# Performance work log

Measured on AMD Instinct MI355X. Metric: run time of the kernel, lower is better.

Reference implementation:

```python
import jax, jax.numpy as jnp
import numpy as np

D_MODEL = 1024
N_HEADS_Q = 16
N_HEADS_KV = 4
D_HEAD = 64  # d_qk = d_v
THETA = 10000.0
CLAMP = 80.0


def apply_rope(x, theta=THETA):
    # x: (b, h, s, d) with d even; interleaved-pair rotary embedding
    b, h, s, d = x.shape
    inv_freq = 1.0 / (theta ** (jnp.arange(0, d, 2, dtype=jnp.float32) / d))  # (d/2,)
    ang = jnp.arange(s, dtype=jnp.float32)[:, None] * inv_freq[None, :]       # (s, d/2)
    cos, sin = jnp.cos(ang), jnp.sin(ang)
    x1, x2 = x[..., 0::2], x[..., 1::2]
    o1 = x1 * cos - x2 * sin
    o2 = x1 * sin + x2 * cos
    return jnp.stack([o1, o2], axis=-1).reshape(b, h, s, d).astype(x.dtype)


def setup_inputs() -> dict:
    key = jax.random.key(0)
    k0, k1, k2, k3, k4 = jax.random.split(key, 5)
    scale = 1.0 / np.sqrt(D_MODEL)
    return {
        "x": jax.random.normal(k0, (2, 2048, D_MODEL), dtype=jnp.float32),
        "Wq": jax.random.normal(k1, (N_HEADS_Q * D_HEAD, D_MODEL), dtype=jnp.float32) * scale,
        "Wk": jax.random.normal(k2, (N_HEADS_KV * D_HEAD, D_MODEL), dtype=jnp.float32) * scale,
        "Wv": jax.random.normal(k3, (N_HEADS_KV * D_HEAD, D_MODEL), dtype=jnp.float32) * scale,
        "Wo": jax.random.normal(k4, (D_MODEL, N_HEADS_Q * D_HEAD), dtype=jnp.float32) * scale,
    }


def _attention(x, Wq, Wk, Wv, Wo):
    b, s, _ = x.shape
    r = N_HEADS_Q // N_HEADS_KV  # queries per KV group
    # projections (Linear: y = x @ W^T, no bias)
    Q = (x @ Wq.T).reshape(b, s, N_HEADS_Q, D_HEAD).transpose(0, 2, 1, 3)   # (b, Hq, s, d)
    K = (x @ Wk.T).reshape(b, s, N_HEADS_KV, D_HEAD).transpose(0, 2, 1, 3)  # (b, Hkv, s, d)
    V = (x @ Wv.T).reshape(b, s, N_HEADS_KV, D_HEAD).transpose(0, 2, 1, 3)
    Q = apply_rope(Q)
    K = apply_rope(K)
    # GQA grouping: (b, Hkv, r, s, d)
    Qg = Q.reshape(b, N_HEADS_KV, r, s, D_HEAD)
    scores = jnp.einsum('bgrqd,bgkd->bgrqk', Qg, K)          # (b, g, r, s, s)
    scores = jnp.clip(scores, -CLAMP, CLAMP)
    causal = jnp.tril(jnp.ones((s, s), dtype=bool))
    scores = jnp.where(causal, scores, -jnp.inf)
    weights = jax.nn.softmax(scores / jnp.sqrt(jnp.float32(D_HEAD)), axis=-1)
    attn = jnp.einsum('bgrqk,bgkd->bgrqd', weights, V)       # (b, g, r, s, d)
    # '... h_kv r s d -> ... s (h_kv r d)'
    attn = attn.transpose(0, 3, 1, 2, 4).reshape(b, s, N_HEADS_Q * D_HEAD)
    return attn @ Wo.T


def reference(x, Wq, Wk, Wv, Wo):
    return _attention(x, Wq, Wk, Wv, Wo)
```

## Files before the change

kernel.cpp:

```cpp
#include <hip/hip_runtime.h>
#include <hip/hip_bf16.h>
#include <math.h>

typedef __attribute__((ext_vector_type(8))) short bf16x8;
typedef __attribute__((ext_vector_type(4))) float f32x4;

#define B_   2
#define S_   2048
#define DM   1024
#define HQ   16
#define HKV  4
#define DH   64

#define MFMA16(a, b, c) __builtin_amdgcn_mfma_f32_16x16x32_bf16(a, b, c, 0, 0, 0)

__device__ __forceinline__ void load_lds16(const __hip_bfloat16* g, __hip_bfloat16* l)
{
    __builtin_amdgcn_global_load_lds(
        (const __attribute__((address_space(1))) unsigned int*)g,
        (__attribute__((address_space(3))) unsigned int*)l, 16, 0, 0);
}

#define CVT_TOTAL 6815744
__global__ void cvt_all(const float* __restrict__ x,  const float* __restrict__ wq,
                        const float* __restrict__ wk, const float* __restrict__ wv,
                        const float* __restrict__ wo,
                        __hip_bfloat16* __restrict__ xb,  __hip_bfloat16* __restrict__ wqb,
                        __hip_bfloat16* __restrict__ wkb, __hip_bfloat16* __restrict__ wvb,
                        __hip_bfloat16* __restrict__ wob)
{
    int i = (blockIdx.x * blockDim.x + threadIdx.x) * 4;
    if (i >= CVT_TOTAL) return;
    const float* src; __hip_bfloat16* dst; int off;
    if      (i < 4194304) { src = x;  dst = xb;  off = 0; }
    else if (i < 5242880) { src = wq; dst = wqb; off = 4194304; }
    else if (i < 5505024) { src = wk; dst = wkb; off = 5242880; }
    else if (i < 5767168) { src = wv; dst = wvb; off = 5505024; }
    else                  { src = wo; dst = wob; off = 5767168; }
    i -= off;
    float4 v = *(const float4*)(src + i);
    union { ushort4 u; __hip_bfloat16 h[4]; } p;
    p.h[0] = __float2bfloat16(v.x);
    p.h[1] = __float2bfloat16(v.y);
    p.h[2] = __float2bfloat16(v.z);
    p.h[3] = __float2bfloat16(v.w);
    *(ushort4*)(dst + i) = p.u;
}

template <bool QKV>
__global__ __launch_bounds__(256, 3) void gemm_tile(
    const __hip_bfloat16* __restrict__ A,
    const __hip_bfloat16* __restrict__ W,
    float* __restrict__ C0, __hip_bfloat16* __restrict__ Qb,
    __hip_bfloat16* __restrict__ Kb, __hip_bfloat16* __restrict__ Vt, int K)
{
    const int wave = threadIdx.x >> 6;
    const int lane = threadIdx.x & 63;
    const int quad = lane >> 4;
    const int l16  = lane & 15;
    const int wm = wave >> 1, wn = wave & 1;
    const int m0 = blockIdx.x * 64;
    const int n0 = blockIdx.y * 128;

    __shared__ __align__(16) __hip_bfloat16 As[2][64 * 64];
    __shared__ __align__(16) __hip_bfloat16 Bs[2][128 * 64];

    f32x4 acc[2][4] = {};

    auto stage = [&](int sb, int kk) {
        #pragma unroll
        for (int r = 0; r < 6; ++r) {
            const int m = wave * 6 + r;
            if (m < 8) {
                const int g = (m << 6) | lane;
                const int row = g >> 3;
                const int cbs = ((g & 7) - row) & 7;
                load_lds16(A + (size_t)(m0 + row) * K + kk + cbs * 8,
                           &As[sb][m * 512]);
            } else {
                const int g = ((m - 8) << 6) | lane;
                const int row = g >> 3;
                const int cbs = ((g & 7) - row) & 7;
                load_lds16(W + (size_t)(n0 + row) * K + kk + cbs * 8,
                           &Bs[sb][(m - 8) * 512]);
            }
        }
    };

    const int NT = K >> 6;
    stage(0, 0);
    __syncthreads();

    for (int t = 0; t < NT; ++t) {
        const int buf = t & 1;
        if (t + 1 < NT) stage(buf ^ 1, (t + 1) << 6);
        #pragma unroll
        for (int ks = 0; ks < 2; ++ks) {
            bf16x8 af[2], bf[4];
            #pragma unroll
            for (int i = 0; i < 2; ++i) {
                const int ra = wm * 32 + i * 16 + l16;
                af[i] = *(const bf16x8*)
                    &As[buf][ra * 64 + ((ks * 4 + quad + ra) & 7) * 8];
            }
            #pragma unroll
            for (int j = 0; j < 4; ++j) {
                const int rb = wn * 64 + j * 16 + l16;
                bf[j] = *(const bf16x8*)
                    &Bs[buf][rb * 64 + ((ks * 4 + quad + rb) & 7) * 8];
            }
            #pragma unroll
            for (int i = 0; i < 2; ++i)
                #pragma unroll
                for (int j = 0; j < 4; ++j)
                    acc[i][j] = MFMA16(af[i], bf[j], acc[i][j]);
        }
        __syncthreads();
    }

    #pragma unroll
    for (int j = 0; j < 4; ++j) {
        const int cbase = n0 + wn * 64 + j * 16;
        const int cb = cbase + l16;
        if (QKV && cbase < 1280) {
            const int ii = (cb >> 1) & 31;
            const float f = exp2f((float)ii * -0.41524101186092f);
            const float f_rev = f * 0.15915494309189535f;
            const bool odd = cb & 1;
            #pragma unroll
            for (int i = 0; i < 2; ++i) {
                #pragma unroll
                for (int reg = 0; reg < 4; ++reg) {
                    const int row = m0 + wm * 32 + i * 16 + quad * 4 + reg;
                    const float v = acc[i][j][reg];
                    const float p = __shfl_xor(v, 1);
                    float rev = (float)(row & (S_ - 1)) * f_rev;
                    rev -= floorf(rev);
                    const float sn = __builtin_amdgcn_sinf(rev);
                    const float cs = __builtin_amdgcn_cosf(rev);
                    const float o = odd ? (p * sn + v * cs) : (v * cs - p * sn);
                    if (cbase < 1024)
                        Qb[(size_t)row * 1024 + cb] = __float2bfloat16(o);
                    else
                        Kb[(size_t)row * 256 + cb - 1024] = __float2bfloat16(o);
                }
            }
        } else {
            #pragma unroll
            for (int i = 0; i < 2; ++i) {
                #pragma unroll
                for (int reg = 0; reg < 4; ++reg) {
                    const int row = m0 + wm * 32 + i * 16 + quad * 4 + reg;
                    const float v = acc[i][j][reg];
                    if (QKV)
                        Vt[((size_t)(row >> 11) * 256 + (cb - 1280)) * S_ +
                           (row & (S_ - 1))] = __float2bfloat16(v);
                    else
                        C0[(size_t)row * 1024 + cb] = v;
                }
            }
        }
    }
}

template <bool MASKED>
__device__ __forceinline__ void softmax_store(
    const f32x4* sacc, int q, int k0, int quad, int l16,
    float& lsum, __hip_bfloat16* PsTile)
{
    #pragma unroll
    for (int nt = 0; nt < 4; ++nt) {
        union { ushort4 u; __hip_bfloat16 h[4]; } pk;
        #pragma unroll
        for (int reg = 0; reg < 4; ++reg) {
            const float sc = fminf(fmaxf(sacc[nt][reg], -80.0f), 80.0f);
            float p = exp2f(fmaf(sc, 0.18033688011112042f,
                                 -14.426950408889634f));
            if (MASKED) {
                const int key = k0 + nt * 16 + quad * 4 + reg;
                p = (key <= q) ? p : 0.0f;
            }
            lsum += p;
            pk.h[reg] = __float2bfloat16(p);
        }
        *(ushort4*)&PsTile[l16 * 72 + nt * 16 + quad * 4] = pk.u;
    }
}

__global__ __launch_bounds__(256, 2) void attn_mfma(
    const __hip_bfloat16* __restrict__ Q,
    const __hip_bfloat16* __restrict__ K,
    const __hip_bfloat16* __restrict__ Vt,
    __hip_bfloat16* __restrict__ ctx)
{
    const int t    = blockIdx.x & 15;
    const int hq   = (blockIdx.x >> 4) & (HQ - 1);
    const int b    = blockIdx.x >> 8;
    const int hkv  = hq >> 2;
    const int wave = threadIdx.x >> 6;
    const int lane = threadIdx.x & 63;
    const int quad = lane >> 4;
    const int l16  = lane & 15;

    const int qlo = t * 64 + wave * 16 + l16;
    const int qhi = (31 - t) * 64 + wave * 16 + l16;

    __shared__ __align__(16) __hip_bfloat16 Ks[2][64 * 64];
    __shared__ __align__(16) __hip_bfloat16 Vs[2][64 * 64];
    __shared__ __align__(16) __hip_bfloat16 Ps[4][2][16 * 72];

    const __hip_bfloat16* qpl = Q + ((size_t)(b * S_) + qlo) * (HQ * DH) + hq * DH + quad * 8;
    const __hip_bfloat16* qph = Q + ((size_t)(b * S_) + qhi) * (HQ * DH) + hq * DH + quad * 8;
    bf16x8 ql0 = *(const bf16x8*)qpl;
    bf16x8 ql1 = *(const bf16x8*)(qpl + 32);
    bf16x8 qh0 = *(const bf16x8*)qph;
    bf16x8 qh1 = *(const bf16x8*)(qph + 32);

    const __hip_bfloat16* Kg = K + (size_t)(b * S_) * (HKV * DH) + hkv * DH;
    const __hip_bfloat16* Vg = Vt + (size_t)(b * HKV + hkv) * DH * S_;

    auto stage = [&](int sb, int k0s) {
        #pragma unroll
        for (int r = 0; r < 2; ++r) {
            const int m = wave * 2 + r;
            const int g = m * 64 + lane;
            const int row = g >> 3;
            const int cbs = ((g & 7) - row) & 7;
            load_lds16(Kg + (size_t)(k0s + row) * (HKV * DH) + cbs * 8, &Ks[sb][m * 512]);
            load_lds16(Vg + (size_t)row * S_ + k0s + cbs * 8, &Vs[sb][m * 512]);
        }
    };

    stage(0, 0);

    float lsum_lo = 0.0f, lsum_hi = 0.0f;
    f32x4 Olo[4] = {}, Ohi[4] = {};
    const f32x4 zro = {0.0f, 0.0f, 0.0f, 0.0f};

    const int last = 31 - t;
    for (int kt = 0; kt <= last; ++kt) {
        const int buf = kt & 1;
        const int k0 = kt * 64;
        __syncthreads();
        if (kt < last) stage(buf ^ 1, k0 + 64);
        const bool dual = (kt <= t);

        bf16x8 ka[4][2];
        #pragma unroll
        for (int nt = 0; nt < 4; ++nt) {
            const int key = nt * 16 + l16;
            ka[nt][0] = *(const bf16x8*)&Ks[buf][key * 64 + ((quad + key) & 7) * 8];
            ka[nt][1] = *(const bf16x8*)&Ks[buf][key * 64 + ((quad + 4 + key) & 7) * 8];
        }
        f32x4 shi[4], slo[4];
        __builtin_amdgcn_s_setprio(1);
        #pragma unroll
        for (int nt = 0; nt < 4; ++nt) {
            shi[nt] = MFMA16(ka[nt][0], qh0, zro);
            shi[nt] = MFMA16(ka[nt][1], qh1, shi[nt]);
        }
        if (dual) {
            #pragma unroll
            for (int nt = 0; nt < 4; ++nt) {
                slo[nt] = MFMA16(ka[nt][0], ql0, zro);
                slo[nt] = MFMA16(ka[nt][1], ql1, slo[nt]);
            }
        }
        __builtin_amdgcn_s_setprio(0);

        if (kt == last) softmax_store<true >(shi, qhi, k0, quad, l16, lsum_hi, &Ps[wave][1][0]);
        else            softmax_store<false>(shi, qhi, k0, quad, l16, lsum_hi, &Ps[wave][1][0]);
        if (dual) {
            if (kt == t) softmax_store<true >(slo, qlo, k0, quad, l16, lsum_lo, &Ps[wave][0][0]);
            else         softmax_store<false>(slo, qlo, k0, quad, l16, lsum_lo, &Ps[wave][0][0]);
        }
        __asm__ __volatile__("s_waitcnt lgkmcnt(0)" ::: "memory");

        bf16x8 va[2][4];
        #pragma unroll
        for (int ks = 0; ks < 2; ++ks)
            #pragma unroll
            for (int dt = 0; dt < 4; ++dt) {
                const int d = dt * 16 + l16;
                va[ks][dt] = *(const bf16x8*)
                    &Vs[buf][d * 64 + ((ks * 4 + quad + d) & 7) * 8];
            }
        __builtin_amdgcn_s_setprio(1);
        #pragma unroll
        for (int ks = 0; ks < 2; ++ks) {
            bf16x8 pb = *(const bf16x8*)&Ps[wave][1][l16 * 72 + ks * 32 + quad * 8];
            #pragma unroll
            for (int dt = 0; dt < 4; ++dt)
                Ohi[dt] = MFMA16(va[ks][dt], pb, Ohi[dt]);
        }
        if (dual) {
            #pragma unroll
            for (int ks = 0; ks < 2; ++ks) {
                bf16x8 pb = *(const bf16x8*)&Ps[wave][0][l16 * 72 + ks * 32 + quad * 8];
                #pragma unroll
                for (int dt = 0; dt < 4; ++dt)
                    Olo[dt] = MFMA16(va[ks][dt], pb, Olo[dt]);
            }
        }
        __builtin_amdgcn_s_setprio(0);
    }

    auto finish = [&](float lsum, const f32x4* O, int qrow) {
        lsum += __shfl_xor(lsum, 16);
        lsum += __shfl_xor(lsum, 32);
        const float inv = 1.0f / lsum;
        __hip_bfloat16* cp =
            ctx + ((size_t)(b * S_) + qrow) * (HQ * DH) + hq * DH + quad * 4;
        #pragma unroll
        for (int dt = 0; dt < 4; ++dt) {
            union { ushort4 u; __hip_bfloat16 h[4]; } o;
            #pragma unroll
            for (int reg = 0; reg < 4; ++reg)
                o.h[reg] = __float2bfloat16(O[dt][reg] * inv);
            *(ushort4*)(cp + dt * 16) = o.u;
        }
    };
    finish(lsum_lo, Olo, qlo);
    finish(lsum_hi, Ohi, qhi);
}

extern "C" void kernel_launch(void* const* d_in, const int* in_sizes, int n_in,
                              void* d_out, int out_size, void* d_ws, size_t ws_size,
                              hipStream_t stream)
{
    const float* x  = (const float*)d_in[0];
    const float* Wq = (const float*)d_in[1];
    const float* Wk = (const float*)d_in[2];
    const float* Wv = (const float*)d_in[3];
    const float* Wo = (const float*)d_in[4];
    float* out = (float*)d_out;

    const int M = B_ * S_;

    char* w = (char*)d_ws;
    __hip_bfloat16* xb    = (__hip_bfloat16*)w;  w += (size_t)M * DM * 2;
    __hip_bfloat16* Wqkvb = (__hip_bfloat16*)w;  w += (size_t)1536 * DM * 2;
    __hip_bfloat16* Wob   = (__hip_bfloat16*)w;  w += (size_t)DM * (HQ * DH) * 2;
    __hip_bfloat16* Qb16  = (__hip_bfloat16*)w;  w += (size_t)M * (HQ * DH) * 2;
    __hip_bfloat16* Kb16  = (__hip_bfloat16*)w;  w += (size_t)M * (HKV * DH) * 2;
    __hip_bfloat16* Vt    = (__hip_bfloat16*)w;  w += (size_t)M * (HKV * DH) * 2;
    __hip_bfloat16* ctx   = (__hip_bfloat16*)w;

    __hip_bfloat16* Wqb = Wqkvb;
    __hip_bfloat16* Wkb = Wqkvb + (size_t)1024 * 1024;
    __hip_bfloat16* Wvb = Wqkvb + (size_t)1280 * 1024;

    cvt_all<<<(CVT_TOTAL / 4 + 255) / 256, 256, 0, stream>>>(
        x, Wq, Wk, Wv, Wo, xb, Wqb, Wkb, Wvb, Wob);

    gemm_tile<true><<<dim3(M / 64, 1536 / 128), 256, 0, stream>>>(
        xb, Wqkvb, nullptr, Qb16, Kb16, Vt, DM);

    attn_mfma<<<B_ * HQ * 16, 256, 0, stream>>>(Qb16, Kb16, Vt, ctx);

    gemm_tile<false><<<dim3(M / 64, 1024 / 128), 256, 0, stream>>>(
        ctx, Wob, out, nullptr, nullptr, nullptr, HQ * DH);
}
```

Before: 168.0 us.

## Replace paired causal query tiles with one tile per block, heaviest-first

```diff
diff --git a/kernel.cpp b/kernel.cpp
--- a/kernel.cpp
+++ b/kernel.cpp
@@ -183,38 +183,38 @@
             lsum += p;
             pk.h[reg] = __float2bfloat16(p);
         }
-        *(ushort4*)&PsTile[l16 * 72 + nt * 16 + quad * 4] = pk.u;
-    }
-}
-
-__global__ __launch_bounds__(256, 2) void attn_mfma(
+        const int g = nt * 2 + (quad >> 1);
+        const int s = (g + l16) & 7;
+        *(ushort4*)&PsTile[l16 * 64 + s * 8 + (quad & 1) * 4] = pk.u;
+    }
+}
+
+__global__ __launch_bounds__(256, 4) void attn_mfma(
     const __hip_bfloat16* __restrict__ Q,
     const __hip_bfloat16* __restrict__ K,
     const __hip_bfloat16* __restrict__ Vt,
     __hip_bfloat16* __restrict__ ctx)
 {
-    const int t    = blockIdx.x & 15;
-    const int hq   = (blockIdx.x >> 4) & (HQ - 1);
-    const int b    = blockIdx.x >> 8;
+    const int jrev = blockIdx.x >> 5;
+    const int j    = 31 - jrev;
+    const int bh   = blockIdx.x & 31;
+    const int b    = bh >> 4;
+    const int hq   = bh & 15;
     const int hkv  = hq >> 2;
     const int wave = threadIdx.x >> 6;
     const int lane = threadIdx.x & 63;
     const int quad = lane >> 4;
     const int l16  = lane & 15;
 
-    const int qlo = t * 64 + wave * 16 + l16;
-    const int qhi = (31 - t) * 64 + wave * 16 + l16;
+    const int q = j * 64 + wave * 16 + l16;
 
     __shared__ __align__(16) __hip_bfloat16 Ks[2][64 * 64];
     __shared__ __align__(16) __hip_bfloat16 Vs[2][64 * 64];
-    __shared__ __align__(16) __hip_bfloat16 Ps[4][2][16 * 72];
-
-    const __hip_bfloat16* qpl = Q + ((size_t)(b * S_) + qlo) * (HQ * DH) + hq * DH + quad * 8;
-    const __hip_bfloat16* qph = Q + ((size_t)(b * S_) + qhi) * (HQ * DH) + hq * DH + quad * 8;
-    bf16x8 ql0 = *(const bf16x8*)qpl;
-    bf16x8 ql1 = *(const bf16x8*)(qpl + 32);
-    bf16x8 qh0 = *(const bf16x8*)qph;
-    bf16x8 qh1 = *(const bf16x8*)(qph + 32);
+    __shared__ __align__(16) __hip_bfloat16 Ps[4][16 * 64];
+
+    const __hip_bfloat16* qp = Q + ((size_t)(b * S_) + q) * (HQ * DH) + hq * DH + quad * 8;
+    bf16x8 q0 = *(const bf16x8*)qp;
+    bf16x8 q1 = *(const bf16x8*)(qp + 32);
 
     const __hip_bfloat16* Kg = K + (size_t)(b * S_) * (HKV * DH) + hkv * DH;
     const __hip_bfloat16* Vg = Vt + (size_t)(b * HKV + hkv) * DH * S_;
@@ -233,17 +233,15 @@
 
     stage(0, 0);
 
-    float lsum_lo = 0.0f, lsum_hi = 0.0f;
-    f32x4 Olo[4] = {}, Ohi[4] = {};
+    float lsum = 0.0f;
+    f32x4 O[4] = {};
     const f32x4 zro = {0.0f, 0.0f, 0.0f, 0.0f};
 
-    const int last = 31 - t;
-    for (int kt = 0; kt <= last; ++kt) {
+    for (int kt = 0; kt <= j; ++kt) {
         const int buf = kt & 1;
         const int k0 = kt * 64;
         __syncthreads();
-        if (kt < last) stage(buf ^ 1, k0 + 64);
-        const bool dual = (kt <= t);
+        if (kt < j) stage(buf ^ 1, k0 + 64);
 
         bf16x8 ka[4][2];
         #pragma unroll
@@ -252,28 +250,17 @@
             ka[nt][0] = *(const bf16x8*)&Ks[buf][key * 64 + ((quad + key) & 7) * 8];
             ka[nt][1] = *(const bf16x8*)&Ks[buf][key * 64 + ((quad + 4 + key) & 7) * 8];
         }
-        f32x4 shi[4], slo[4];
+        f32x4 s[4];
         __builtin_amdgcn_s_setprio(1);
         #pragma unroll
         for (int nt = 0; nt < 4; ++nt) {
-            shi[nt] = MFMA16(ka[nt][0], qh0, zro);
-            shi[nt] = MFMA16(ka[nt][1], qh1, shi[nt]);
-        }
-        if (dual) {
-            #pragma unroll
-            for (int nt = 0; nt < 4; ++nt) {
-                slo[nt] = MFMA16(ka[nt][0], ql0, zro);
-                slo[nt] = MFMA16(ka[nt][1], ql1, slo[nt]);
-            }
+            s[nt] = MFMA16(ka[nt][0], q0, zro);
+            s[nt] = MFMA16(ka[nt][1], q1, s[nt]);
         }
         __builtin_amdgcn_s_setprio(0);
 
-        if (kt == last) softmax_store<true >(shi, qhi, k0, quad, l16, lsum_hi, &Ps[wave][1][0]);
-        else            softmax_store<false>(shi, qhi, k0, quad, l16, lsum_hi, &Ps[wave][1][0]);
-        if (dual) {
-            if (kt == t) softmax_store<true >(slo, qlo, k0, quad, l16, lsum_lo, &Ps[wave][0][0]);
-            else         softmax_store<false>(slo, qlo, k0, quad, l16, lsum_lo, &Ps[wave][0][0]);
-        }
+        if (kt == j) softmax_store<true >(s, q, k0, quad, l16, lsum, &Ps[wave][0]);
+        else         softmax_store<false>(s, q, k0, quad, l16, lsum, &Ps[wave][0]);
         __asm__ __volatile__("s_waitcnt lgkmcnt(0)" ::: "memory");
 
         bf16x8 va[2][4];
@@ -288,40 +275,28 @@
         __builtin_amdgcn_s_setprio(1);
         #pragma unroll
         for (int ks = 0; ks < 2; ++ks) {
-            bf16x8 pb = *(const bf16x8*)&Ps[wave][1][l16 * 72 + ks * 32 + quad * 8];
+            bf16x8 pb = *(const bf16x8*)
+                &Ps[wave][l16 * 64 + ((ks * 4 + quad + l16) & 7) * 8];
             #pragma unroll
             for (int dt = 0; dt < 4; ++dt)
-                Ohi[dt] = MFMA16(va[ks][dt], pb, Ohi[dt]);
-        }
-        if (dual) {
-            #pragma unroll
-            for (int ks = 0; ks < 2; ++ks) {
-                bf16x8 pb = *(const bf16x8*)&Ps[wave][0][l16 * 72 + ks * 32 + quad * 8];
-                #pragma unroll
-                for (int dt = 0; dt < 4; ++dt)
-                    Olo[dt] = MFMA16(va[ks][dt], pb, Olo[dt]);
-            }
+                O[dt] = MFMA16(va[ks][dt], pb, O[dt]);
         }
         __builtin_amdgcn_s_setprio(0);
     }
 
-    auto finish = [&](float lsum, const f32x4* O, int qrow) {
-        lsum += __shfl_xor(lsum, 16);
-        lsum += __shfl_xor(lsum, 32);
-        const float inv = 1.0f / lsum;
-        __hip_bfloat16* cp =
-            ctx + ((size_t)(b * S_) + qrow) * (HQ * DH) + hq * DH + quad * 4;
-        #pragma unroll
-        for (int dt = 0; dt < 4; ++dt) {
-            union { ushort4 u; __hip_bfloat16 h[4]; } o;
-            #pragma unroll
-            for (int reg = 0; reg < 4; ++reg)
-                o.h[reg] = __float2bfloat16(O[dt][reg] * inv);
-            *(ushort4*)(cp + dt * 16) = o.u;
-        }
-    };
-    finish(lsum_lo, Olo, qlo);
-    finish(lsum_hi, Ohi, qhi);
+    lsum += __shfl_xor(lsum, 16);
+    lsum += __shfl_xor(lsum, 32);
+    const float inv = 1.0f / lsum;
+    __hip_bfloat16* cp =
+        ctx + ((size_t)(b * S_) + q) * (HQ * DH) + hq * DH + quad * 4;
+    #pragma unroll
+    for (int dt = 0; dt < 4; ++dt) {
+        union { ushort4 u; __hip_bfloat16 h[4]; } o;
+        #pragma unroll
+        for (int reg = 0; reg < 4; ++reg)
+            o.h[reg] = __float2bfloat16(O[dt][reg] * inv);
+        *(ushort4*)(cp + dt * 16) = o.u;
+    }
 }
 
 extern "C" void kernel_launch(void* const* d_in, const int* in_sizes, int n_in,
@@ -356,7 +331,7 @@
     gemm_tile<true><<<dim3(M / 64, 1536 / 128), 256, 0, stream>>>(
         xb, Wqkvb, nullptr, Qb16, Kb16, Vt, DM);
 
-    attn_mfma<<<B_ * HQ * 16, 256, 0, stream>>>(Qb16, Kb16, Vt, ctx);
+    attn_mfma<<<B_ * HQ * 32, 256, 0, stream>>>(Qb16, Kb16, Vt, ctx);
 
     gemm_tile<false><<<dim3(M / 64, 1024 / 128), 256, 0, stream>>>(
         ctx, Wob, out, nullptr, nullptr, nullptr, HQ * DH);
```

After: 160.2 us. 4.6% less time.
